# Performance work log

Measured on AMD Instinct MI355X. Metric: run time of the kernel, lower is better.

## Reference

```python
import jax, jax.numpy as jnp
import numpy as np

INPUT_DIM = 768
OUTPUT_DIM = 768
GRID_SIZE = 5
BATCH = 8192


def setup_inputs() -> dict:
    key = jax.random.key(0)
    k1, k2 = jax.random.split(key)
    x = jax.random.normal(k1, (BATCH, INPUT_DIM), dtype=jnp.float32)
    coeffs = jax.random.normal(k2, (INPUT_DIM, OUTPUT_DIM, GRID_SIZE), dtype=jnp.float32) * 0.1
    scale = jnp.ones((INPUT_DIM, OUTPUT_DIM), dtype=jnp.float32)
    shift = jnp.zeros((INPUT_DIM, OUTPUT_DIM), dtype=jnp.float32)
    return {"x": x, "coeffs": coeffs, "scale": scale, "shift": shift}


def reference(x, coeffs, scale, shift):
    # x: [B, I]; coeffs: [I, J, G]; scale/shift: [I, J]
    grid = jnp.linspace(-1.0, 1.0, GRID_SIZE, dtype=x.dtype)        # [G]
    x_norm = jnp.tanh(x)                                            # [B, I]
    # RBF basis: exp(-5 * (x_norm - grid)^2) -> [B, I, G]
    basis = jnp.exp(-5.0 * (x_norm[:, :, None] - grid) ** 2)
    # Fold scale into coeffs, contract over input dim and grid:
    # out[b,j] = sum_{i,g} basis[b,i,g] * coeffs[i,j,g] * scale[i,j] + sum_i shift[i,j]
    w = coeffs * scale[:, :, None]                                  # [I, J, G]
    out = jnp.einsum('big,ijg->bj', basis, w)                       # [B, J]
    out = out + jnp.sum(shift, axis=0)                              # broadcast bias [J]
    return out
```

## Files before the change

kernel.cpp:

```cpp
#include <hip/hip_runtime.h>
#include <hip/hip_bf16.h>
#include <cstdint>
#include <cstddef>

#define BATCH 8192
#define IDIM  768
#define JDIM  768
#define GRID  5
#define KDIM  (IDIM * GRID)


__device__ __forceinline__ unsigned short f2bf(float f) {
    unsigned int u = __float_as_uint(f);
    u += 0x7fffu + ((u >> 16) & 1u);
    return (unsigned short)(u >> 16);
}

typedef __bf16 bf16x8 __attribute__((ext_vector_type(8)));
typedef float  f32x4  __attribute__((ext_vector_type(4)));
typedef unsigned short ushortx4 __attribute__((ext_vector_type(4)));

__device__ __forceinline__ void async_copy16(const void* gsrc, void* ldsdst) {
    __builtin_amdgcn_global_load_lds(
        (const __attribute__((address_space(1))) unsigned int*)gsrc,
        (__attribute__((address_space(3))) unsigned int*)ldsdst,
        16, 0, 0);
}


#define WT_I 32
#define WT_J 64

__global__ __launch_bounds__(256)
void wt_bias_kernel(const float* __restrict__ coeffs,
                    const float* __restrict__ scale,
                    const float* __restrict__ shift,
                    unsigned short* __restrict__ Wt,
                    float* __restrict__ bias) {
    __shared__ __align__(16) unsigned short tile[GRID][WT_J][WT_I + 4];
    __shared__ float red[4][WT_J];
    const int t  = threadIdx.x;
    const int i0 = (blockIdx.x / (JDIM / WT_J)) * WT_I;
    const int j0 = (blockIdx.x % (JDIM / WT_J)) * WT_J;
    const int jj = t & 63;

    float ssum = 0.f;
#pragma unroll
    for (int it = 0; it < (WT_I * WT_J) / 256; ++it) {
        const int ii = it * 4 + (t >> 6);
        const int i = i0 + ii, j = j0 + jj;
        const float* cp = &coeffs[((size_t)i * JDIM + j) * GRID];
        const float  sc = scale[(size_t)i * JDIM + j];
        ssum += shift[(size_t)i * JDIM + j];
#pragma unroll
        for (int g = 0; g < GRID; ++g)
            tile[g][jj][ii] = f2bf(cp[g] * sc);
    }
    red[t >> 6][jj] = ssum;
    __syncthreads();
    if (t < WT_J)
        atomicAdd(&bias[j0 + t], red[0][t] + red[1][t] + red[2][t] + red[3][t]);

#pragma unroll
    for (int it = 0; it < (WT_J * GRID * (WT_I / 4)) / 256; ++it) {
        const int p  = it * 256 + t;
        const int iq = p & 7;
        const int q  = p >> 3;
        const int g  = q % GRID;
        const int j  = q / GRID;
        ushortx4 v = *(const ushortx4*)&tile[g][j][iq * 4];
        *(ushortx4*)&Wt[(size_t)(j0 + j) * KDIM + g * IDIM + i0 + iq * 4] = v;
    }
}


__global__ __launch_bounds__(256)
void basis_kernel(const float* __restrict__ x, unsigned short* __restrict__ Abas) {
    const int idx = blockIdx.x * 256 + threadIdx.x;
    const int b  = idx / (IDIM / 4);
    const int i4 = (idx - b * (IDIM / 4)) * 4;
    const float4 xv = *(const float4*)&x[(size_t)b * IDIM + i4];
    const float xs[4] = {xv.x, xv.y, xv.z, xv.w};
    float tv[4];
#pragma unroll
    for (int u = 0; u < 4; ++u) {
        const float e = __expf(2.f * xs[u]);
        tv[u] = 1.f - 2.f / (e + 1.f);
    }
#pragma unroll
    for (int g = 0; g < GRID; ++g) {
        const float gv = -1.f + 0.5f * (float)g;
        ushortx4 o;
#pragma unroll
        for (int u = 0; u < 4; ++u) {
            const float d = tv[u] - gv;
            o[u] = f2bf(__expf(-5.f * d * d));
        }
        *(ushortx4*)&Abas[(size_t)b * KDIM + g * IDIM + i4] = o;
    }
}


#define BM 128
#define BN 96
#define BK 64
#define KT (KDIM / BK)

__global__ __launch_bounds__(256, 2)
void kan_gemm(const unsigned short* __restrict__ Abas,
              const unsigned short* __restrict__ Wt,
              const float* __restrict__ bias,
              float* __restrict__ out) {
    __shared__ unsigned short As[3][BM * BK];
    __shared__ unsigned short Bs[2][BN * BK];

    const int t    = threadIdx.x;
    const int lane = t & 63;
    const int wave = t >> 6;
    const int m0 = blockIdx.x * BM;
    const int n0 = blockIdx.y * BN;
    const int wm = (wave >> 1) * 64;
    const int wn = (wave & 1) * 48;

    f32x4 acc[4][3] = {};

    const int lrow = t >> 3;
    const int lc   = t & 7;
    const int cg   = lc ^ (lrow & 7);
    const int ldsoff = lrow * BK + lc * 8;
    const size_t abase = (size_t)(m0 + lrow) * KDIM + cg * 8;
    const size_t bbase = (size_t)(n0 + lrow) * KDIM + cg * 8;

    auto stage_a = [&](int buf, int kt_el) {
#pragma unroll
        for (int s = 0; s < 4; ++s)
            async_copy16(&Abas[abase + (size_t)(32 * s) * KDIM + kt_el],
                         &As[buf][ldsoff + 32 * s * BK]);
    };
    auto stage_b = [&](int buf, int kt_el) {
#pragma unroll
        for (int s = 0; s < 3; ++s)
            async_copy16(&Wt[bbase + (size_t)(32 * s) * KDIM + kt_el],
                         &Bs[buf][ldsoff + 32 * s * BK]);
    };

    auto compute_tile = [&](int ab, int bb) {
#pragma unroll
        for (int ks = 0; ks < 2; ++ks) {
            const int pc = ((ks * 4) + (lane >> 4)) ^ (lane & 7);
            bf16x8 af[4], bfr[3];
#pragma unroll
            for (int f = 0; f < 4; ++f)
                af[f]  = *(const bf16x8*)&As[ab][(wm + f * 16 + (lane & 15)) * BK + pc * 8];
#pragma unroll
            for (int f = 0; f < 3; ++f)
                bfr[f] = *(const bf16x8*)&Bs[bb][(wn + f * 16 + (lane & 15)) * BK + pc * 8];
#pragma unroll
            for (int fm = 0; fm < 4; ++fm)
#pragma unroll
                for (int fn = 0; fn < 3; ++fn)
                    acc[fm][fn] = __builtin_amdgcn_mfma_f32_16x16x32_bf16(
                        af[fm], bfr[fn], acc[fm][fn], 0, 0, 0);
        }
    };

    stage_a(0, 0);
    stage_a(1, BK);
    stage_b(0, 0);

    int ac = 0, a2 = 2;
    for (int tt = 0; tt < KT - 2; ++tt) {
        stage_a(a2, (tt + 2) * BK);
        stage_b((tt + 1) & 1, (tt + 1) * BK);
        asm volatile("s_waitcnt vmcnt(7)" ::: "memory");
        __builtin_amdgcn_s_barrier();
        __builtin_amdgcn_sched_barrier(0);
        compute_tile(ac, tt & 1);
        __builtin_amdgcn_s_barrier();
        ac = (ac == 2) ? 0 : ac + 1;
        a2 = (a2 == 2) ? 0 : a2 + 1;
    }
    {
        const int tt = KT - 2;
        stage_b((tt + 1) & 1, (tt + 1) * BK);
        asm volatile("s_waitcnt vmcnt(3)" ::: "memory");
        __builtin_amdgcn_s_barrier();
        __builtin_amdgcn_sched_barrier(0);
        compute_tile(ac, tt & 1);
        __builtin_amdgcn_s_barrier();
        ac = (ac == 2) ? 0 : ac + 1;
    }
    {
        const int tt = KT - 1;
        asm volatile("s_waitcnt vmcnt(0)" ::: "memory");
        __builtin_amdgcn_s_barrier();
        __builtin_amdgcn_sched_barrier(0);
        compute_tile(ac, tt & 1);
    }

    const int col   = lane & 15;
    const int rbase = (lane >> 4) * 4;
#pragma unroll
    for (int fm = 0; fm < 4; ++fm) {
#pragma unroll
        for (int fn = 0; fn < 3; ++fn) {
            const int j  = n0 + wn + fn * 16 + col;
            const float bj = bias[j];
#pragma unroll
            for (int r = 0; r < 4; ++r) {
                const int row = m0 + wm + fm * 16 + rbase + r;
                out[(size_t)row * JDIM + j] = acc[fm][fn][r] + bj;
            }
        }
    }
}


__global__ __launch_bounds__(256)
void fallback_kernel(const float* __restrict__ x,
                     const float* __restrict__ coeffs,
                     const float* __restrict__ scale,
                     const float* __restrict__ shift,
                     float* __restrict__ out) {
    __shared__ float bas[KDIM];
    const int b = blockIdx.x;
    const int t = threadIdx.x;
    for (int i = t; i < IDIM; i += 256) {
        float tv = tanhf(x[(size_t)b * IDIM + i]);
#pragma unroll
        for (int g = 0; g < GRID; ++g) {
            float d = tv - (-1.0f + 0.5f * (float)g);
            bas[g * IDIM + i] = __expf(-5.0f * d * d);
        }
    }
    __syncthreads();
#pragma unroll
    for (int jj = 0; jj < 3; ++jj) {
        const int j = t + jj * 256;
        float acc = 0.f;
        for (int i = 0; i < IDIM; ++i) {
            const float sc = scale[(size_t)i * JDIM + j];
            const float* cp = &coeffs[((size_t)i * JDIM + j) * GRID];
            float s5 = 0.f;
#pragma unroll
            for (int g = 0; g < GRID; ++g) s5 += bas[g * IDIM + i] * cp[g];
            acc += s5 * sc + shift[(size_t)i * JDIM + j];
        }
        out[(size_t)b * JDIM + j] = acc;
    }
}


extern "C" void kernel_launch(void* const* d_in, const int* in_sizes, int n_in,
                              void* d_out, int out_size, void* d_ws, size_t ws_size,
                              hipStream_t stream) {
    const float* x      = (const float*)d_in[0];
    const float* coeffs = (const float*)d_in[1];
    const float* scale  = (const float*)d_in[2];
    const float* shift  = (const float*)d_in[3];
    float* out = (float*)d_out;

    const size_t wt_bytes   = (size_t)JDIM * KDIM * sizeof(unsigned short);
    const size_t bias_off   = wt_bytes;
    const size_t bias_bytes = (size_t)JDIM * sizeof(float);
    const size_t bas_off    = bias_off + bias_bytes;
    const size_t bas_bytes  = (size_t)BATCH * KDIM * sizeof(unsigned short);
    const size_t need       = bas_off + bas_bytes;

    if (ws_size >= need) {
        unsigned short* Wt   = (unsigned short*)d_ws;
        float*          bias = (float*)((char*)d_ws + bias_off);
        unsigned short* Abas = (unsigned short*)((char*)d_ws + bas_off);

        hipMemsetAsync(bias, 0, bias_bytes, stream);
        wt_bias_kernel<<<(IDIM / WT_I) * (JDIM / WT_J), 256, 0, stream>>>(coeffs, scale, shift, Wt, bias);
        basis_kernel<<<(BATCH * (IDIM / 4)) / 256, 256, 0, stream>>>(x, Abas);
        kan_gemm<<<dim3(BATCH / BM, JDIM / BN), 256, 0, stream>>>(Abas, Wt, bias, out);
    } else {
        fallback_kernel<<<BATCH, 256, 0, stream>>>(x, coeffs, scale, shift, out);
    }
}
```

Measured before the change: 157.3 us.

## Pre-swizzle weights into MFMA fragment layout and load B directly to registers

The weight prep kernel now writes Wt in an MFMA-fragment-ordered layout, so each lane's bf16x8 B fragment sits contiguously in global memory. The GEMM drops the LDS staging buffer for B and double-buffers B fragments in registers via direct global loads issued one tile ahead. The main loop is unrolled by two to ping-pong the register buffers. This removes LDS traffic and LDS space for B, at the cost of more VGPRs and of each wave reloading B from L2/global instead of sharing it through LDS.

```diff
diff --git a/kernel.cpp b/kernel.cpp
--- a/kernel.cpp
+++ b/kernel.cpp
@@ -30,12 +30,14 @@
 
 #define WT_I 32
 #define WT_J 64
+#define NJF  (JDIM / 16)
+#define NKS  (KDIM / 32)
 
 __global__ __launch_bounds__(256)
 void wt_bias_kernel(const float* __restrict__ coeffs,
                     const float* __restrict__ scale,
                     const float* __restrict__ shift,
-                    unsigned short* __restrict__ Wt,
+                    unsigned short* __restrict__ Wt3,
                     float* __restrict__ bias) {
     __shared__ __align__(16) unsigned short tile[GRID][WT_J][WT_I + 4];
     __shared__ float red[4][WT_J];
@@ -62,14 +64,19 @@
         atomicAdd(&bias[j0 + t], red[0][t] + red[1][t] + red[2][t] + red[3][t]);
 
 #pragma unroll
-    for (int it = 0; it < (WT_J * GRID * (WT_I / 4)) / 256; ++it) {
-        const int p  = it * 256 + t;
-        const int iq = p & 7;
-        const int q  = p >> 3;
-        const int g  = q % GRID;
-        const int j  = q / GRID;
-        ushortx4 v = *(const ushortx4*)&tile[g][j][iq * 4];
-        *(ushortx4*)&Wt[(size_t)(j0 + j) * KDIM + g * IDIM + i0 + iq * 4] = v;
+    for (int it = 0; it < 10; ++it) {
+        const int s    = it * 256 + t;
+        const int h    = s & 1;
+        const int lane = (s >> 1) & 63;
+        const int q    = s >> 7;
+        const int jf_l = q & 3;
+        const int g    = q >> 2;
+        const int i_loc = (lane >> 4) * 8 + h * 4;
+        const int j_loc = jf_l * 16 + (lane & 15);
+        ushortx4 v = *(const ushortx4*)&tile[g][j_loc][i_loc];
+        const int ks  = g * (IDIM / 32) + (i0 >> 5);
+        const int jfg = (j0 >> 4) + jf_l;
+        *(ushortx4*)&Wt3[((((size_t)ks * NJF + jfg) * 64 + lane) * 8) + h * 4] = v;
     }
 }
 
@@ -108,11 +115,10 @@
 
 __global__ __launch_bounds__(256, 2)
 void kan_gemm(const unsigned short* __restrict__ Abas,
-              const unsigned short* __restrict__ Wt,
+              const unsigned short* __restrict__ Wt3,
               const float* __restrict__ bias,
               float* __restrict__ out) {
     __shared__ unsigned short As[3][BM * BK];
-    __shared__ unsigned short Bs[2][BN * BK];
 
     const int t    = threadIdx.x;
     const int lane = t & 63;
@@ -129,7 +135,6 @@
     const int cg   = lc ^ (lrow & 7);
     const int ldsoff = lrow * BK + lc * 8;
     const size_t abase = (size_t)(m0 + lrow) * KDIM + cg * 8;
-    const size_t bbase = (size_t)(n0 + lrow) * KDIM + cg * 8;
 
     auto stage_a = [&](int buf, int kt_el) {
 #pragma unroll
@@ -137,65 +142,78 @@
             async_copy16(&Abas[abase + (size_t)(32 * s) * KDIM + kt_el],
                          &As[buf][ldsoff + 32 * s * BK]);
     };
-    auto stage_b = [&](int buf, int kt_el) {
-#pragma unroll
-        for (int s = 0; s < 3; ++s)
-            async_copy16(&Wt[bbase + (size_t)(32 * s) * KDIM + kt_el],
-                         &Bs[buf][ldsoff + 32 * s * BK]);
+
+    const unsigned short* bp0 = Wt3 + (((size_t)((n0 + wn) >> 4) * 64 + lane) * 8);
+    auto load_b = [&](int tt, bf16x8 (&dst)[6]) {
+        const unsigned short* bp = bp0 + (size_t)(tt * 2) * (NJF * 512);
+#pragma unroll
+        for (int ks = 0; ks < 2; ++ks)
+#pragma unroll
+            for (int f = 0; f < 3; ++f)
+                dst[ks * 3 + f] = *(const bf16x8*)&bp[(size_t)ks * (NJF * 512) + f * 512];
     };
 
-    auto compute_tile = [&](int ab, int bb) {
+    auto compute_tile = [&](int ab, const bf16x8 (&bfr)[6]) {
 #pragma unroll
         for (int ks = 0; ks < 2; ++ks) {
             const int pc = ((ks * 4) + (lane >> 4)) ^ (lane & 7);
-            bf16x8 af[4], bfr[3];
+            bf16x8 af[4];
 #pragma unroll
             for (int f = 0; f < 4; ++f)
-                af[f]  = *(const bf16x8*)&As[ab][(wm + f * 16 + (lane & 15)) * BK + pc * 8];
-#pragma unroll
-            for (int f = 0; f < 3; ++f)
-                bfr[f] = *(const bf16x8*)&Bs[bb][(wn + f * 16 + (lane & 15)) * BK + pc * 8];
+                af[f] = *(const bf16x8*)&As[ab][(wm + f * 16 + (lane & 15)) * BK + pc * 8];
 #pragma unroll
             for (int fm = 0; fm < 4; ++fm)
 #pragma unroll
                 for (int fn = 0; fn < 3; ++fn)
                     acc[fm][fn] = __builtin_amdgcn_mfma_f32_16x16x32_bf16(
-                        af[fm], bfr[fn], acc[fm][fn], 0, 0, 0);
+                        af[fm], bfr[ks * 3 + fn], acc[fm][fn], 0, 0, 0);
         }
     };
+
+    bf16x8 b0[6], b1[6];
 
     stage_a(0, 0);
     stage_a(1, BK);
-    stage_b(0, 0);
+    load_b(0, b0);
 
     int ac = 0, a2 = 2;
-    for (int tt = 0; tt < KT - 2; ++tt) {
+#pragma unroll 1
+    for (int p = 0; p < (KT - 2) / 2; ++p) {
+        int tt = 2 * p;
         stage_a(a2, (tt + 2) * BK);
-        stage_b((tt + 1) & 1, (tt + 1) * BK);
-        asm volatile("s_waitcnt vmcnt(7)" ::: "memory");
+        load_b(tt + 1, b1);
+        asm volatile("s_waitcnt vmcnt(10)" ::: "memory");
         __builtin_amdgcn_s_barrier();
         __builtin_amdgcn_sched_barrier(0);
-        compute_tile(ac, tt & 1);
+        compute_tile(ac, b0);
         __builtin_amdgcn_s_barrier();
         ac = (ac == 2) ? 0 : ac + 1;
         a2 = (a2 == 2) ? 0 : a2 + 1;
+        ++tt;
+        stage_a(a2, (tt + 2) * BK);
+        load_b(tt + 1, b0);
+        asm volatile("s_waitcnt vmcnt(10)" ::: "memory");
+        __builtin_amdgcn_s_barrier();
+        __builtin_amdgcn_sched_barrier(0);
+        compute_tile(ac, b1);
+        __builtin_amdgcn_s_barrier();
+        ac = (ac == 2) ? 0 : ac + 1;
+        a2 = (a2 == 2) ? 0 : a2 + 1;
     }
     {
-        const int tt = KT - 2;
-        stage_b((tt + 1) & 1, (tt + 1) * BK);
-        asm volatile("s_waitcnt vmcnt(3)" ::: "memory");
+        load_b(KT - 1, b1);
+        asm volatile("s_waitcnt vmcnt(6)" ::: "memory");
         __builtin_amdgcn_s_barrier();
         __builtin_amdgcn_sched_barrier(0);
-        compute_tile(ac, tt & 1);
+        compute_tile(ac, b0);
         __builtin_amdgcn_s_barrier();
         ac = (ac == 2) ? 0 : ac + 1;
     }
     {
-        const int tt = KT - 1;
         asm volatile("s_waitcnt vmcnt(0)" ::: "memory");
         __builtin_amdgcn_s_barrier();
         __builtin_amdgcn_sched_barrier(0);
-        compute_tile(ac, tt & 1);
+        compute_tile(ac, b1);
     }
 
     const int col   = lane & 15;
@@ -268,14 +286,14 @@
     const size_t need       = bas_off + bas_bytes;
 
     if (ws_size >= need) {
-        unsigned short* Wt   = (unsigned short*)d_ws;
+        unsigned short* Wt3  = (unsigned short*)d_ws;
         float*          bias = (float*)((char*)d_ws + bias_off);
         unsigned short* Abas = (unsigned short*)((char*)d_ws + bas_off);
 
         hipMemsetAsync(bias, 0, bias_bytes, stream);
-        wt_bias_kernel<<<(IDIM / WT_I) * (JDIM / WT_J), 256, 0, stream>>>(coeffs, scale, shift, Wt, bias);
+        wt_bias_kernel<<<(IDIM / WT_I) * (JDIM / WT_J), 256, 0, stream>>>(coeffs, scale, shift, Wt3, bias);
         basis_kernel<<<(BATCH * (IDIM / 4)) / 256, 256, 0, stream>>>(x, Abas);
-        kan_gemm<<<dim3(BATCH / BM, JDIM / BN), 256, 0, stream>>>(Abas, Wt, bias, out);
+        kan_gemm<<<dim3(BATCH / BM, JDIM / BN), 256, 0, stream>>>(Abas, Wt3, bias, out);
     } else {
         fallback_kernel<<<BATCH, 256, 0, stream>>>(x, coeffs, scale, shift, out);
     }
```

Result: faster. 152.8 us (-2.8%).
